# Kernel optimization log

Hardware: AMD Instinct MI355X
Metric: run time of the kernel (lower is better)

Reference implementation:

```python
import jax, jax.numpy as jnp
import numpy as np

D_MODEL = 2048
NUM_HEADS = 32
NUM_GROUPS = 8
D_K = D_MODEL // NUM_HEADS          # 64
GROUP_SIZE = NUM_HEADS // NUM_GROUPS  # 4


def setup_inputs() -> dict:
    key = jax.random.key(0)
    ks = jax.random.split(key, 7)
    B, S = 2, 2048
    x = jax.random.normal(ks[0], (B, S, D_MODEL), dtype=jnp.float32)
    sc = 1.0 / np.sqrt(D_MODEL)
    Wq = jax.random.normal(ks[1], (D_MODEL, D_MODEL), dtype=jnp.float32) * sc
    bq = jax.random.normal(ks[2], (D_MODEL,), dtype=jnp.float32) * 0.01
    Wk = jax.random.normal(ks[3], (D_MODEL, D_K * NUM_GROUPS), dtype=jnp.float32) * sc
    bk = jax.random.normal(ks[4], (D_K * NUM_GROUPS,), dtype=jnp.float32) * 0.01
    Wv = jax.random.normal(ks[5], (D_MODEL, D_K * NUM_GROUPS), dtype=jnp.float32) * sc
    bv = jax.random.normal(ks[6], (D_K * NUM_GROUPS,), dtype=jnp.float32) * 0.01
    return {"x": x, "Wq": Wq, "bq": bq, "Wk": Wk, "bk": bk, "Wv": Wv, "bv": bv}


def reference(x, Wq, bq, Wk, bk, Wv, bv):
    B, S, D = x.shape
    # q: (B, G, gs, S, dk)
    q = (x @ Wq + bq).reshape(B, S, NUM_HEADS, D_K).transpose(0, 2, 1, 3)
    q = q.reshape(B, NUM_GROUPS, GROUP_SIZE, S, D_K)
    # k, v: (B, G, S, dk)
    k = (x @ Wk + bk).reshape(B, S, NUM_GROUPS, D_K).transpose(0, 2, 1, 3)
    v = (x @ Wv + bv).reshape(B, S, NUM_GROUPS, D_K).transpose(0, 2, 1, 3)
    # scores: (B, G, gs, S_q, S_k)
    scores = jnp.einsum('bgqsd,bgtd->bgqst', q, k) / (D_K ** 0.5)
    attn = jax.nn.softmax(scores, axis=-1)
    out = jnp.einsum('bgqst,bgtd->bgqsd', attn, v)  # (B, G, gs, S, dk)
    # Faithful to source: transpose(1,2) then view(B, S, -1) (scrambles seq axis)
    out = out.transpose(0, 2, 1, 3, 4).reshape(B, S, -1)
    return out
```

## Files before the change

kernel.cpp:

```cpp
#include <hip/hip_runtime.h>

typedef _Float16 f16;
typedef _Float16 half8 __attribute__((ext_vector_type(8)));
typedef _Float16 half4v __attribute__((ext_vector_type(4)));
typedef __fp16 fp16x2 __attribute__((ext_vector_type(2)));
typedef float floatx4 __attribute__((ext_vector_type(4)));
typedef float f32x16 __attribute__((ext_vector_type(16)));
typedef unsigned uint4v __attribute__((ext_vector_type(4)));

#define GLL16(g, l) __builtin_amdgcn_global_load_lds( \
    (const __attribute__((address_space(1))) void*)(g), \
    (__attribute__((address_space(3))) void*)(l), 16, 0, 0)

static __device__ __forceinline__ float pairsum(float x) {
    return x + __shfl_xor(x, 32);
}
static __device__ __forceinline__ unsigned pkh(float a, float b) {
    fp16x2 h = __builtin_amdgcn_cvt_pkrtz(a, b);
    return __builtin_bit_cast(unsigned, h);
}

__global__ __launch_bounds__(256) void cvt_x_kernel(const float* __restrict__ x,
                                                    f16* __restrict__ xh) {
    size_t i = ((size_t)blockIdx.x * 256 + threadIdx.x) * 8;
    float4 a = *(const float4*)(x + i);
    float4 b = *(const float4*)(x + i + 4);
    half8 h;
    h[0] = (f16)a.x; h[1] = (f16)a.y; h[2] = (f16)a.z; h[3] = (f16)a.w;
    h[4] = (f16)b.x; h[5] = (f16)b.y; h[6] = (f16)b.z; h[7] = (f16)b.w;
    *(half8*)(xh + i) = h;
}

__global__ __launch_bounds__(256) void wt_kernel(const float* __restrict__ Wq,
                                                 const float* __restrict__ Wk,
                                                 const float* __restrict__ Wv,
                                                 f16* __restrict__ Wt) {
    __shared__ float tile[64][65];
    int n0 = (blockIdx.x % 48) * 64;
    int k0 = (blockIdx.x / 48) * 64;
    const float* src; int ld, c0;
    if (n0 < 2048)      { src = Wq; ld = 2048; c0 = n0; }
    else if (n0 < 2560) { src = Wk; ld = 512;  c0 = n0 - 2048; }
    else                { src = Wv; ld = 512;  c0 = n0 - 2560; }
    int t = threadIdx.x;
    #pragma unroll
    for (int i = 0; i < 16; ++i) {
        int idx = t + i * 256;
        int r = idx >> 6, c = idx & 63;
        tile[r][c] = src[(size_t)(k0 + r) * ld + c0 + c];
    }
    __syncthreads();
    #pragma unroll
    for (int i = 0; i < 2; ++i) {
        int idx = t + i * 256;
        int nr = idx >> 3, kc = (idx & 7) * 8;
        half8 h;
        #pragma unroll
        for (int j = 0; j < 8; ++j) h[j] = (f16)tile[kc + j][nr];
        *(half8*)(Wt + (size_t)(n0 + nr) * 2048 + k0 + kc) = h;
    }
}

__global__ __launch_bounds__(256) void qkv_gemm_kernel(
    const f16* __restrict__ A, const f16* __restrict__ Bt,
    const float* __restrict__ bq, const float* __restrict__ bk, const float* __restrict__ bv,
    f16* __restrict__ Qb, f16* __restrict__ Kb, f16* __restrict__ Vt) {
    __shared__ f16 As[128 * 64];
    __shared__ f16 Bs[128 * 64];
    const int K = 2048;
    int bid = blockIdx.x;
    int j5 = bid >> 3;
    int tm = (bid & 7) + 8 * (j5 / 24);
    int tn = j5 % 24;
    int m0 = tm * 128, n0 = tn * 128;
    int tid = threadIdx.x, lane = tid & 63, wid = tid >> 6;
    int wr = wid >> 1, wc = wid & 1;
    int lr = lane & 15, lg = lane >> 4;
    floatx4 acc[4][4] = {};

    int lrow = wid * 8 + (lane >> 3);
    int lcol = (((lane & 7) ^ ((lane >> 3) & 7)) * 8);
    char* AsB = (char*)As;
    char* BsB = (char*)Bs;
    int rsw = (lr & 7) << 4;

    for (int kt = 0; kt < K; kt += 64) {
        __syncthreads();
        #pragma unroll
        for (int i = 0; i < 4; ++i) {
            GLL16(A  + (size_t)(m0 + i * 32 + lrow) * K + kt + lcol, AsB + i * 4096 + wid * 1024);
            GLL16(Bt + (size_t)(n0 + i * 32 + lrow) * K + kt + lcol, BsB + i * 4096 + wid * 1024);
        }
        __syncthreads();
        #pragma unroll
        for (int ks = 0; ks < 2; ++ks) {
            half8 af[4], bf[4];
            #pragma unroll
            for (int i = 0; i < 4; ++i)
                af[i] = *(const half8*)(AsB + (wr * 64 + i * 16 + lr) * 128 + ((ks * 64 + lg * 16) ^ rsw));
            #pragma unroll
            for (int i = 0; i < 4; ++i)
                bf[i] = *(const half8*)(BsB + (wc * 64 + i * 16 + lr) * 128 + ((ks * 64 + lg * 16) ^ rsw));
            #pragma unroll
            for (int i = 0; i < 4; ++i)
                #pragma unroll
                for (int jj = 0; jj < 4; ++jj)
                    acc[i][jj] = __builtin_amdgcn_mfma_f32_16x16x32_f16(bf[jj], af[i], acc[i][jj], 0, 0, 0);
        }
    }

    int b = m0 >> 11;
    #pragma unroll
    for (int jj = 0; jj < 4; ++jj) {
        int nb = n0 + wc * 64 + jj * 16 + lg * 4;
        if (nb < 2048) {
            int hcol = nb >> 6, d0 = nb & 63;
            float4 bias4 = *(const float4*)(bq + nb);
            f16* dstb = Qb + (size_t)(b * 32 + hcol) * 131072 + d0;
            #pragma unroll
            for (int i = 0; i < 4; ++i) {
                int s = (m0 + wr * 64 + i * 16 + lr) & 2047;
                half4v hv;
                hv[0] = (f16)(acc[i][jj][0] + bias4.x);
                hv[1] = (f16)(acc[i][jj][1] + bias4.y);
                hv[2] = (f16)(acc[i][jj][2] + bias4.z);
                hv[3] = (f16)(acc[i][jj][3] + bias4.w);
                *(half4v*)(dstb + (size_t)s * 64) = hv;
            }
        } else if (nb < 2560) {
            int nk = nb - 2048;
            int gg = nk >> 6, d0 = nk & 63;
            float4 bias4 = *(const float4*)(bk + nk);
            f16* dstb = Kb + (size_t)(b * 8 + gg) * 131072 + d0;
            #pragma unroll
            for (int i = 0; i < 4; ++i) {
                int s = (m0 + wr * 64 + i * 16 + lr) & 2047;
                half4v hv;
                hv[0] = (f16)(acc[i][jj][0] + bias4.x);
                hv[1] = (f16)(acc[i][jj][1] + bias4.y);
                hv[2] = (f16)(acc[i][jj][2] + bias4.z);
                hv[3] = (f16)(acc[i][jj][3] + bias4.w);
                *(half4v*)(dstb + (size_t)s * 64) = hv;
            }
        } else {
            int nv = nb - 2560;
            int gg = nv >> 6, d0 = nv & 63;
            float4 bias4 = *(const float4*)(bv + nv);
            f16* dstb = Vt + (size_t)((b * 8 + gg) * 64 + d0) * 2048;
            #pragma unroll
            for (int i = 0; i < 4; ++i) {
                int s = (m0 + wr * 64 + i * 16 + lr) & 2047;
                int sp = (s & ~12) | ((s & 4) << 1) | ((s & 8) >> 1);
                dstb[sp]            = (f16)(acc[i][jj][0] + bias4.x);
                dstb[2048 + sp]     = (f16)(acc[i][jj][1] + bias4.y);
                dstb[4096 + sp]     = (f16)(acc[i][jj][2] + bias4.z);
                dstb[6144 + sp]     = (f16)(acc[i][jj][3] + bias4.w);
            }
        }
    }
}

__global__ __launch_bounds__(128, 2) void attn_kernel(
    const f16* __restrict__ Qb, const f16* __restrict__ Kb, const f16* __restrict__ Vt,
    float* __restrict__ out) {
    __shared__ __align__(16) f16 Kl[2][64 * 64];
    __shared__ __align__(16) f16 Vl[2][64 * 64];

    int bid = blockIdx.x;
    int hh = (bid & 7) * 8 + ((bid >> 3) & 7);
    int qb = bid >> 6;
    int b = hh >> 5, h = hh & 31, g = h >> 2, qh = h & 3;
    int tid = threadIdx.x, lane = tid & 63, wid = tid >> 6;
    int lc = lane & 31, hi = lane >> 5;

    const f16* Qhead = Qb + (size_t)(b * 32 + h) * 131072;
    const f16* Khead = Kb + (size_t)(b * 8 + g) * 131072;
    const f16* Vhead = Vt + (size_t)(b * 8 + g) * 131072;
    int q0 = qb * 128 + wid * 64;
    int sqA = q0 + lc, sqB = q0 + 32 + lc;

    half8 qfA[4], qfB[4];
    #pragma unroll
    for (int ks = 0; ks < 4; ++ks) {
        qfA[ks] = *(const half8*)(Qhead + (size_t)sqA * 64 + ks * 16 + hi * 8);
        qfB[ks] = *(const half8*)(Qhead + (size_t)sqB * 64 + ks * 16 + hi * 8);
    }

    f32x16 ocA0 = {}, ocA1 = {}, ocB0 = {}, ocB1 = {};
    float lA = 0.f, lB = 0.f;
    const float SC = 0.125f * 1.44269504088896f;
    const float MSH = 5.770780163555851f;

    int r_ = wid * 32 + (lane >> 3);
    int csx = ((lane & 7) ^ (r_ & 7)) * 8;
    char* KlB = (char*)Kl;
    char* VlB = (char*)Vl;

    int ro0 = lc * 128, ro1 = (lc + 32) * 128;
    int sw = (lc & 7) << 4;

    #pragma unroll
    for (int i = 0; i < 4; ++i) {
        GLL16(Khead + (size_t)(r_ + i * 8) * 64 + csx,        KlB + wid * 4096 + i * 1024);
        GLL16(Vhead + (size_t)(r_ + i * 8) * 2048 + csx,      VlB + wid * 4096 + i * 1024);
    }
    __syncthreads();

    #pragma unroll 1
    for (int t = 0; t < 32; ++t) {
        int c = t & 1;
        char* KB = KlB + c * 8192;
        char* VB = VlB + c * 8192;
        if (t < 31) {
            int nk = (t + 1) * 64;
            #pragma unroll
            for (int i = 0; i < 4; ++i) {
                GLL16(Khead + (size_t)(nk + r_ + i * 8) * 64 + csx,
                      KlB + (c ^ 1) * 8192 + wid * 4096 + i * 1024);
                GLL16(Vhead + (size_t)(r_ + i * 8) * 2048 + nk + csx,
                      VlB + (c ^ 1) * 8192 + wid * 4096 + i * 1024);
            }
        }

        f32x16 sA0 = {}, sA1 = {}, sB0 = {}, sB1 = {};
        __builtin_amdgcn_s_setprio(1);
        #pragma unroll
        for (int ks = 0; ks < 4; ++ks) {
            half8 kf0 = *(const half8*)(KB + ((ro0 + ks * 32 + hi * 16) ^ sw));
            half8 kf1 = *(const half8*)(KB + ((ro1 + ks * 32 + hi * 16) ^ sw));
            sA0 = __builtin_amdgcn_mfma_f32_32x32x16_f16(kf0, qfA[ks], sA0, 0, 0, 0);
            sA1 = __builtin_amdgcn_mfma_f32_32x32x16_f16(kf1, qfA[ks], sA1, 0, 0, 0);
        }
        #pragma unroll
        for (int ks = 0; ks < 4; ++ks) {
            half8 kf0 = *(const half8*)(KB + ((ro0 + ks * 32 + hi * 16) ^ sw));
            half8 kf1 = *(const half8*)(KB + ((ro1 + ks * 32 + hi * 16) ^ sw));
            sB0 = __builtin_amdgcn_mfma_f32_32x32x16_f16(kf0, qfB[ks], sB0, 0, 0, 0);
            sB1 = __builtin_amdgcn_mfma_f32_32x32x16_f16(kf1, qfB[ks], sB1, 0, 0, 0);
        }
        __builtin_amdgcn_s_setprio(0);

        float rsA = 0.f;
        #pragma unroll
        for (int r = 0; r < 16; ++r) {
            float pa0 = __builtin_amdgcn_exp2f(fmaf(sA0[r], SC, -MSH));
            float pa1 = __builtin_amdgcn_exp2f(fmaf(sA1[r], SC, -MSH));
            sA0[r] = pa0; sA1[r] = pa1;
            rsA += pa0 + pa1;
        }
        lA += rsA;

        #pragma unroll
        for (int tt = 0; tt < 2; ++tt) {
            #pragma unroll
            for (int ks2 = 0; ks2 < 2; ++ks2) {
                int base = ks2 * 8;
                uint4v uA;
                if (tt == 0) {
                    uA[0] = pkh(sA0[base + 0], sA0[base + 1]);
                    uA[1] = pkh(sA0[base + 2], sA0[base + 3]);
                    uA[2] = pkh(sA0[base + 4], sA0[base + 5]);
                    uA[3] = pkh(sA0[base + 6], sA0[base + 7]);
                } else {
                    uA[0] = pkh(sA1[base + 0], sA1[base + 1]);
                    uA[1] = pkh(sA1[base + 2], sA1[base + 3]);
                    uA[2] = pkh(sA1[base + 4], sA1[base + 5]);
                    uA[3] = pkh(sA1[base + 6], sA1[base + 7]);
                }
                half8 pA = __builtin_bit_cast(half8, uA);
                int cb = tt * 64 + ks2 * 32 + hi * 16;
                half8 vf0 = *(const half8*)(VB + ((ro0 + cb) ^ sw));
                half8 vf1 = *(const half8*)(VB + ((ro1 + cb) ^ sw));
                ocA0 = __builtin_amdgcn_mfma_f32_32x32x16_f16(vf0, pA, ocA0, 0, 0, 0);
                ocA1 = __builtin_amdgcn_mfma_f32_32x32x16_f16(vf1, pA, ocA1, 0, 0, 0);
            }
        }

        float rsB = 0.f;
        #pragma unroll
        for (int r = 0; r < 16; ++r) {
            float pb0 = __builtin_amdgcn_exp2f(fmaf(sB0[r], SC, -MSH));
            float pb1 = __builtin_amdgcn_exp2f(fmaf(sB1[r], SC, -MSH));
            sB0[r] = pb0; sB1[r] = pb1;
            rsB += pb0 + pb1;
        }
        lB += rsB;

        #pragma unroll
        for (int tt = 0; tt < 2; ++tt) {
            #pragma unroll
            for (int ks2 = 0; ks2 < 2; ++ks2) {
                int base = ks2 * 8;
                uint4v uB;
                if (tt == 0) {
                    uB[0] = pkh(sB0[base + 0], sB0[base + 1]);
                    uB[1] = pkh(sB0[base + 2], sB0[base + 3]);
                    uB[2] = pkh(sB0[base + 4], sB0[base + 5]);
                    uB[3] = pkh(sB0[base + 6], sB0[base + 7]);
                } else {
                    uB[0] = pkh(sB1[base + 0], sB1[base + 1]);
                    uB[1] = pkh(sB1[base + 2], sB1[base + 3]);
                    uB[2] = pkh(sB1[base + 4], sB1[base + 5]);
                    uB[3] = pkh(sB1[base + 6], sB1[base + 7]);
                }
                half8 pB = __builtin_bit_cast(half8, uB);
                int cb = tt * 64 + ks2 * 32 + hi * 16;
                half8 vf0 = *(const half8*)(VB + ((ro0 + cb) ^ sw));
                half8 vf1 = *(const half8*)(VB + ((ro1 + cb) ^ sw));
                ocB0 = __builtin_amdgcn_mfma_f32_32x32x16_f16(vf0, pB, ocB0, 0, 0, 0);
                ocB1 = __builtin_amdgcn_mfma_f32_32x32x16_f16(vf1, pB, ocB1, 0, 0, 0);
            }
        }
        __syncthreads();
    }

    lA = pairsum(lA); lB = pairsum(lB);
    float invA = 1.f / lA, invB = 1.f / lB;
    size_t obase = (size_t)b * 4194304 + (size_t)(qh * 8 + g) * 131072 + hi * 4;
    size_t obA = obase + (size_t)sqA * 64;
    size_t obB = obase + (size_t)sqB * 64;
    #pragma unroll
    for (int rg = 0; rg < 4; ++rg) {
        floatx4 vA0, vA1, vB0, vB1;
        #pragma unroll
        for (int j = 0; j < 4; ++j) {
            vA0[j] = ocA0[rg * 4 + j] * invA;
            vA1[j] = ocA1[rg * 4 + j] * invA;
            vB0[j] = ocB0[rg * 4 + j] * invB;
            vB1[j] = ocB1[rg * 4 + j] * invB;
        }
        *(floatx4*)(out + obA + rg * 8) = vA0;
        *(floatx4*)(out + obA + 32 + rg * 8) = vA1;
        *(floatx4*)(out + obB + rg * 8) = vB0;
        *(floatx4*)(out + obB + 32 + rg * 8) = vB1;
    }
}

extern "C" void kernel_launch(void* const* d_in, const int* in_sizes, int n_in,
                              void* d_out, int out_size, void* d_ws, size_t ws_size,
                              hipStream_t stream) {
    const float* x  = (const float*)d_in[0];
    const float* Wq = (const float*)d_in[1];
    const float* bq = (const float*)d_in[2];
    const float* Wk = (const float*)d_in[3];
    const float* bk = (const float*)d_in[4];
    const float* Wv = (const float*)d_in[5];
    const float* bv = (const float*)d_in[6];
    float* out = (float*)d_out;

    char* ws = (char*)d_ws;
    f16* xh = (f16*)ws;
    f16* Wt = (f16*)(ws + 16777216);
    f16* Qb = (f16*)(ws + 29360128);
    f16* Kb = (f16*)(ws + 46137344);
    f16* Vt = (f16*)(ws + 50331648);

    cvt_x_kernel<<<4096, 256, 0, stream>>>(x, xh);
    wt_kernel<<<1536, 256, 0, stream>>>(Wq, Wk, Wv, Wt);
    qkv_gemm_kernel<<<768, 256, 0, stream>>>(xh, Wt, bq, bk, bv, Qb, Kb, Vt);
    attn_kernel<<<1024, 128, 0, stream>>>(Qb, Kb, Vt, out);
}
```

Measured before the change: 183.1 us.

## Rewrite QKV GEMM with 256x256 tiles and double-buffered ping-pong pipeline

The QKV projection GEMM moves from 128x128 tiles with 256 threads and a single LDS buffer to 256x256 tiles with 512 threads (8 waves) and a double-buffered 128KB LDS. The main loop interleaves global-to-LDS staging of the next k-tile with MFMA quadrants, using explicit waitcnt, barriers, sched_barrier and s_setprio so that loads hide behind matrix math. The larger tile also increases operand reuse per byte loaded. In exchange, the grid shrinks to 192 blocks, which may leave some compute units idle. Register pressure and LDS occupancy also rise to one block per CU.

```diff
diff --git a/kernel.cpp b/kernel.cpp
--- a/kernel.cpp
+++ b/kernel.cpp
@@ -61,70 +61,144 @@
     }
 }
 
-__global__ __launch_bounds__(256) void qkv_gemm_kernel(
+__global__ __launch_bounds__(512, 2) void qkv_gemm_kernel(
     const f16* __restrict__ A, const f16* __restrict__ Bt,
     const float* __restrict__ bq, const float* __restrict__ bk, const float* __restrict__ bv,
     f16* __restrict__ Qb, f16* __restrict__ Kb, f16* __restrict__ Vt) {
-    __shared__ f16 As[128 * 64];
-    __shared__ f16 Bs[128 * 64];
+    __shared__ __align__(16) char SM[131072];
     const int K = 2048;
     int bid = blockIdx.x;
-    int j5 = bid >> 3;
-    int tm = (bid & 7) + 8 * (j5 / 24);
-    int tn = j5 % 24;
-    int m0 = tm * 128, n0 = tn * 128;
+    int rg8 = bid & 7, j = bid >> 3;
+    int tm = (rg8 >> 1) * 4 + j / 6;
+    int tn = (rg8 & 1) * 6 + j % 6;
+    int m0 = tm * 256, n0 = tn * 256;
     int tid = threadIdx.x, lane = tid & 63, wid = tid >> 6;
-    int wr = wid >> 1, wc = wid & 1;
+    int wr = wid >> 2, wc = wid & 3;
     int lr = lane & 15, lg = lane >> 4;
-    floatx4 acc[4][4] = {};
-
-    int lrow = wid * 8 + (lane >> 3);
-    int lcol = (((lane & 7) ^ ((lane >> 3) & 7)) * 8);
-    char* AsB = (char*)As;
-    char* BsB = (char*)Bs;
+    floatx4 acc[8][4] = {};
+    half8 af[4][2], bf[4][2];
+
+    int srow = tid >> 3;
+    int scol = ((tid & 7) ^ (srow & 7)) * 8;
     int rsw = (lr & 7) << 4;
-
-    for (int kt = 0; kt < K; kt += 64) {
-        __syncthreads();
-        #pragma unroll
-        for (int i = 0; i < 4; ++i) {
-            GLL16(A  + (size_t)(m0 + i * 32 + lrow) * K + kt + lcol, AsB + i * 4096 + wid * 1024);
-            GLL16(Bt + (size_t)(n0 + i * 32 + lrow) * K + kt + lcol, BsB + i * 4096 + wid * 1024);
-        }
-        __syncthreads();
-        #pragma unroll
-        for (int ks = 0; ks < 2; ++ks) {
-            half8 af[4], bf[4];
-            #pragma unroll
-            for (int i = 0; i < 4; ++i)
-                af[i] = *(const half8*)(AsB + (wr * 64 + i * 16 + lr) * 128 + ((ks * 64 + lg * 16) ^ rsw));
-            #pragma unroll
-            for (int i = 0; i < 4; ++i)
-                bf[i] = *(const half8*)(BsB + (wc * 64 + i * 16 + lr) * 128 + ((ks * 64 + lg * 16) ^ rsw));
-            #pragma unroll
-            for (int i = 0; i < 4; ++i)
-                #pragma unroll
-                for (int jj = 0; jj < 4; ++jj)
-                    acc[i][jj] = __builtin_amdgcn_mfma_f32_16x16x32_f16(bf[jj], af[i], acc[i][jj], 0, 0, 0);
-        }
-    }
+    char* SMb = (char*)SM;
+    char* Abuf0 = SMb;
+    char* Abuf1 = SMb + 32768;
+    char* Bbuf0 = SMb + 65536;
+    char* Bbuf1 = SMb + 98304;
+
+#define STAGE_A(t, p) GLL16(A + (size_t)(m0 + (p) * 64 + srow) * K + (t) * 64 + scol, \
+                            SMb + ((t) & 1) * 32768 + (p) * 8192 + (wid << 10))
+#define STAGE_B(t, p) GLL16(Bt + (size_t)(n0 + (p) * 64 + srow) * K + (t) * 64 + scol, \
+                            SMb + 65536 + ((t) & 1) * 32768 + (p) * 8192 + (wid << 10))
+#define LOAD_B(bufp)                                                          \
+    _Pragma("unroll") for (int nj = 0; nj < 4; ++nj)                          \
+    _Pragma("unroll") for (int ks = 0; ks < 2; ++ks)                          \
+        bf[nj][ks] = *(const half8*)((bufp) + (wc * 64 + nj * 16 + lr) * 128  \
+                                     + ((ks * 64 + lg * 16) ^ rsw));
+#define LOAD_A(bufp, qh)                                                      \
+    _Pragma("unroll") for (int mi = 0; mi < 4; ++mi)                          \
+    _Pragma("unroll") for (int ks = 0; ks < 2; ++ks)                          \
+        af[mi][ks] = *(const half8*)((bufp) + (wr * 128 + ((qh) * 4 + mi) * 16 + lr) * 128 \
+                                     + ((ks * 64 + lg * 16) ^ rsw));
+#define MMA_Q(qh, ql)                                                         \
+    _Pragma("unroll") for (int mi = 0; mi < 4; ++mi)                          \
+    _Pragma("unroll") for (int nj = 0; nj < 2; ++nj)                          \
+    _Pragma("unroll") for (int ks = 0; ks < 2; ++ks)                          \
+        acc[(qh) * 4 + mi][(ql) * 2 + nj] = __builtin_amdgcn_mfma_f32_16x16x32_f16( \
+            bf[(ql) * 2 + nj][ks], af[mi][ks], acc[(qh) * 4 + mi][(ql) * 2 + nj], 0, 0, 0);
+
+    STAGE_A(0, 0); STAGE_A(0, 1); STAGE_A(0, 2); STAGE_A(0, 3);
+    STAGE_B(0, 0); STAGE_B(0, 1); STAGE_B(0, 2); STAGE_B(0, 3);
+
+    #pragma unroll 1
+    for (int i = 0; i < 16; ++i) {
+        int t1 = 2 * i + 1, t2 = 2 * i + 2;
+        STAGE_A(t1, 0); STAGE_A(t1, 1);
+        asm volatile("s_waitcnt vmcnt(2)" ::: "memory");
+        __builtin_amdgcn_s_barrier();
+        __builtin_amdgcn_sched_barrier(0);
+        LOAD_B(Bbuf0); LOAD_A(Abuf0, 0);
+        asm volatile("s_waitcnt lgkmcnt(0)" ::: "memory");
+        __builtin_amdgcn_sched_barrier(0);
+        __builtin_amdgcn_s_setprio(1);
+        MMA_Q(0, 0);
+        __builtin_amdgcn_s_setprio(0);
+        __builtin_amdgcn_s_barrier();
+        STAGE_A(t1, 2); STAGE_A(t1, 3);
+        __builtin_amdgcn_s_setprio(1);
+        MMA_Q(0, 1);
+        __builtin_amdgcn_s_setprio(0);
+        __builtin_amdgcn_s_barrier();
+        LOAD_A(Abuf0, 1);
+        STAGE_B(t1, 0); STAGE_B(t1, 1);
+        asm volatile("s_waitcnt lgkmcnt(0)" ::: "memory");
+        __builtin_amdgcn_sched_barrier(0);
+        __builtin_amdgcn_s_setprio(1);
+        MMA_Q(1, 0);
+        __builtin_amdgcn_s_setprio(0);
+        __builtin_amdgcn_s_barrier();
+        STAGE_B(t1, 2); STAGE_B(t1, 3);
+        __builtin_amdgcn_s_setprio(1);
+        MMA_Q(1, 1);
+        __builtin_amdgcn_s_setprio(0);
+        __builtin_amdgcn_s_barrier();
+        if (i < 15) {
+            STAGE_A(t2, 0); STAGE_A(t2, 1);
+            asm volatile("s_waitcnt vmcnt(2)" ::: "memory");
+        } else {
+            asm volatile("s_waitcnt vmcnt(0)" ::: "memory");
+        }
+        __builtin_amdgcn_s_barrier();
+        __builtin_amdgcn_sched_barrier(0);
+        LOAD_B(Bbuf1); LOAD_A(Abuf1, 0);
+        asm volatile("s_waitcnt lgkmcnt(0)" ::: "memory");
+        __builtin_amdgcn_sched_barrier(0);
+        __builtin_amdgcn_s_setprio(1);
+        MMA_Q(0, 0);
+        __builtin_amdgcn_s_setprio(0);
+        __builtin_amdgcn_s_barrier();
+        if (i < 15) { STAGE_A(t2, 2); STAGE_A(t2, 3); }
+        __builtin_amdgcn_s_setprio(1);
+        MMA_Q(0, 1);
+        __builtin_amdgcn_s_setprio(0);
+        __builtin_amdgcn_s_barrier();
+        LOAD_A(Abuf1, 1);
+        if (i < 15) { STAGE_B(t2, 0); STAGE_B(t2, 1); }
+        asm volatile("s_waitcnt lgkmcnt(0)" ::: "memory");
+        __builtin_amdgcn_sched_barrier(0);
+        __builtin_amdgcn_s_setprio(1);
+        MMA_Q(1, 0);
+        __builtin_amdgcn_s_setprio(0);
+        __builtin_amdgcn_s_barrier();
+        if (i < 15) { STAGE_B(t2, 2); STAGE_B(t2, 3); }
+        __builtin_amdgcn_s_setprio(1);
+        MMA_Q(1, 1);
+        __builtin_amdgcn_s_setprio(0);
+        __builtin_amdgcn_s_barrier();
+    }
+#undef STAGE_A
+#undef STAGE_B
+#undef LOAD_A
+#undef LOAD_B
+#undef MMA_Q
 
     int b = m0 >> 11;
     #pragma unroll
-    for (int jj = 0; jj < 4; ++jj) {
-        int nb = n0 + wc * 64 + jj * 16 + lg * 4;
+    for (int nj = 0; nj < 4; ++nj) {
+        int nb = n0 + wc * 64 + nj * 16 + lg * 4;
         if (nb < 2048) {
             int hcol = nb >> 6, d0 = nb & 63;
             float4 bias4 = *(const float4*)(bq + nb);
             f16* dstb = Qb + (size_t)(b * 32 + hcol) * 131072 + d0;
             #pragma unroll
-            for (int i = 0; i < 4; ++i) {
-                int s = (m0 + wr * 64 + i * 16 + lr) & 2047;
+            for (int mi = 0; mi < 8; ++mi) {
+                int s = (m0 + wr * 128 + mi * 16 + lr) & 2047;
                 half4v hv;
-                hv[0] = (f16)(acc[i][jj][0] + bias4.x);
-                hv[1] = (f16)(acc[i][jj][1] + bias4.y);
-                hv[2] = (f16)(acc[i][jj][2] + bias4.z);
-                hv[3] = (f16)(acc[i][jj][3] + bias4.w);
+                hv[0] = (f16)(acc[mi][nj][0] + bias4.x);
+                hv[1] = (f16)(acc[mi][nj][1] + bias4.y);
+                hv[2] = (f16)(acc[mi][nj][2] + bias4.z);
+                hv[3] = (f16)(acc[mi][nj][3] + bias4.w);
                 *(half4v*)(dstb + (size_t)s * 64) = hv;
             }
         } else if (nb < 2560) {
@@ -133,13 +207,13 @@
             float4 bias4 = *(const float4*)(bk + nk);
             f16* dstb = Kb + (size_t)(b * 8 + gg) * 131072 + d0;
             #pragma unroll
-            for (int i = 0; i < 4; ++i) {
-                int s = (m0 + wr * 64 + i * 16 + lr) & 2047;
+            for (int mi = 0; mi < 8; ++mi) {
+                int s = (m0 + wr * 128 + mi * 16 + lr) & 2047;
                 half4v hv;
-                hv[0] = (f16)(acc[i][jj][0] + bias4.x);
-                hv[1] = (f16)(acc[i][jj][1] + bias4.y);
-                hv[2] = (f16)(acc[i][jj][2] + bias4.z);
-                hv[3] = (f16)(acc[i][jj][3] + bias4.w);
+                hv[0] = (f16)(acc[mi][nj][0] + bias4.x);
+                hv[1] = (f16)(acc[mi][nj][1] + bias4.y);
+                hv[2] = (f16)(acc[mi][nj][2] + bias4.z);
+                hv[3] = (f16)(acc[mi][nj][3] + bias4.w);
                 *(half4v*)(dstb + (size_t)s * 64) = hv;
             }
         } else {
@@ -148,13 +222,13 @@
             float4 bias4 = *(const float4*)(bv + nv);
             f16* dstb = Vt + (size_t)((b * 8 + gg) * 64 + d0) * 2048;
             #pragma unroll
-            for (int i = 0; i < 4; ++i) {
-                int s = (m0 + wr * 64 + i * 16 + lr) & 2047;
+            for (int mi = 0; mi < 8; ++mi) {
+                int s = (m0 + wr * 128 + mi * 16 + lr) & 2047;
                 int sp = (s & ~12) | ((s & 4) << 1) | ((s & 8) >> 1);
-                dstb[sp]            = (f16)(acc[i][jj][0] + bias4.x);
-                dstb[2048 + sp]     = (f16)(acc[i][jj][1] + bias4.y);
-                dstb[4096 + sp]     = (f16)(acc[i][jj][2] + bias4.z);
-                dstb[6144 + sp]     = (f16)(acc[i][jj][3] + bias4.w);
+                dstb[sp]        = (f16)(acc[mi][nj][0] + bias4.x);
+                dstb[2048 + sp] = (f16)(acc[mi][nj][1] + bias4.y);
+                dstb[4096 + sp] = (f16)(acc[mi][nj][2] + bias4.z);
+                dstb[6144 + sp] = (f16)(acc[mi][nj][3] + bias4.w);
             }
         }
     }
@@ -323,11 +397,11 @@
     for (int rg = 0; rg < 4; ++rg) {
         floatx4 vA0, vA1, vB0, vB1;
         #pragma unroll
-        for (int j = 0; j < 4; ++j) {
-            vA0[j] = ocA0[rg * 4 + j] * invA;
-            vA1[j] = ocA1[rg * 4 + j] * invA;
-            vB0[j] = ocB0[rg * 4 + j] * invB;
-            vB1[j] = ocB1[rg * 4 + j] * invB;
+        for (int jj = 0; jj < 4; ++jj) {
+            vA0[jj] = ocA0[rg * 4 + jj] * invA;
+            vA1[jj] = ocA1[rg * 4 + jj] * invA;
+            vB0[jj] = ocB0[rg * 4 + jj] * invB;
+            vB1[jj] = ocB1[rg * 4 + jj] * invB;
         }
         *(floatx4*)(out + obA + rg * 8) = vA0;
         *(floatx4*)(out + obA + 32 + rg * 8) = vA1;
@@ -357,6 +431,6 @@
 
     cvt_x_kernel<<<4096, 256, 0, stream>>>(x, xh);
     wt_kernel<<<1536, 256, 0, stream>>>(Wq, Wk, Wv, Wt);
-    qkv_gemm_kernel<<<768, 256, 0, stream>>>(xh, Wt, bq, bk, bv, Qb, Kb, Vt);
+    qkv_gemm_kernel<<<192, 512, 0, stream>>>(xh, Wt, bq, bk, bv, Qb, Kb, Vt);
     attn_kernel<<<1024, 128, 0, stream>>>(Qb, Kb, Vt, out);
 }
```

New measurement: 160.1 us. -12.6%, faster.
